# Performance work log

Hardware: AMD Instinct MI355X
Metric: run time of the kernel (lower is better)

## Reference

```python
import jax, jax.numpy as jnp
import numpy as np

B, S, D, H = 2, 2048, 1024, 16
DH = D // H


def setup_inputs() -> dict:
    key = jax.random.key(0)
    ks = jax.random.split(key, 5)
    scale = 0.02
    return {
        "X": jax.random.normal(ks[0], (B, S, D), jnp.float32),
        "Wq": jax.random.normal(ks[1], (H, D, DH), jnp.float32) * scale,
        "Wk": jax.random.normal(ks[2], (H, D, DH), jnp.float32) * scale,
        "Wv": jax.random.normal(ks[3], (H, D, DH), jnp.float32) * scale,
        "Wo": jax.random.normal(ks[4], (D, D), jnp.float32) * scale,
        "bo": jnp.zeros((D,), jnp.float32),
    }


def reference(X, Wq, Wk, Wv, Wo, bo):
    # Per-head projections, batched over heads: [B,H,S,DH]
    Q = jnp.einsum('bsd,hde->bhse', X, Wq)
    K = jnp.einsum('bsd,hde->bhse', X, Wk)
    V = jnp.einsum('bsd,hde->bhse', X, Wv)
    # Scores scaled by sqrt(d_model) exactly as in the source (not sqrt(d_head))
    A = jnp.einsum('bhse,bhte->bhst', Q, K) / jnp.sqrt(jnp.float32(D))
    A = jax.nn.softmax(A, axis=-1)  # no mask in the source
    O = jnp.einsum('bhst,bhte->bhse', A, V)  # [B,H,S,DH]
    # Concat heads -> [B,S,D], then output projection
    O = jnp.transpose(O, (0, 2, 1, 3)).reshape(B, S, D)
    return O @ Wo + bo
```

## Files before the change

### kernel.cpp

```cpp
#include <hip/hip_runtime.h>
#include <math.h>

static constexpr int Bc  = 2;
static constexpr int Sc  = 2048;
static constexpr int Dc  = 1024;
static constexpr int Hc  = 16;
static constexpr int DHc = 64;

typedef short bf16x8 __attribute__((ext_vector_type(8)));
typedef float f32x4  __attribute__((ext_vector_type(4)));

static constexpr float LOG2E = 1.4426950408889634f;

static __device__ __forceinline__ unsigned short f2bf(float x) {
  union { float f; unsigned u; } v; v.f = x;
  unsigned r = v.u + 0x7FFFu + ((v.u >> 16) & 1u);
  return (unsigned short)(r >> 16);
}
static __device__ __forceinline__ float bf2f(unsigned short u) {
  union { unsigned u; float f; } v; v.u = ((unsigned)u) << 16;
  return v.f;
}
static __device__ __forceinline__ unsigned pk2bf_trunc(float a, float b) {
  return __builtin_amdgcn_perm(__float_as_uint(b), __float_as_uint(a), 0x07060302u);
}
#if __has_builtin(__builtin_amdgcn_exp2f)
#define EXP2F(x) __builtin_amdgcn_exp2f(x)
#else
#define EXP2F(x) exp2f(x)
#endif

static __device__ __forceinline__ void gload16(const void* g, void* l) {
  __builtin_amdgcn_global_load_lds(
      (const __attribute__((address_space(1))) void*)g,
      (__attribute__((address_space(3))) void*)l, 16, 0, 0);
}

__global__ __launch_bounds__(256) void prep(
    const float* __restrict__ Wq, const float* __restrict__ Wk,
    const float* __restrict__ Wv, const float* __restrict__ Wo,
    const float* __restrict__ X,
    unsigned short* __restrict__ Wt3, unsigned short* __restrict__ Wot,
    unsigned short* __restrict__ Xb) {
  const int z = blockIdx.z;
  if (z == 4) {
    size_t base = ((size_t)blockIdx.y * 16 + blockIdx.x) * 4096;
#pragma unroll
    for (int it = 0; it < 16; ++it) {
      size_t i = base + it * 256 + threadIdx.x;
      float4 v = ((const float4*)X)[i];
      ushort4 u; u.x = f2bf(v.x); u.y = f2bf(v.y); u.z = f2bf(v.z); u.w = f2bf(v.w);
      ((ushort4*)Xb)[i] = u;
    }
    return;
  }
  __shared__ unsigned short T[64][68];
  const float* src; unsigned short* dst;
  int srcld, dstld, r0, c0;
  if (z < 3) {
    const float* W = (z == 0) ? Wq : (z == 1) ? Wk : Wv;
    unsigned short* Wt = Wt3 + (size_t)z * Dc * Dc;
    int h = blockIdx.y;
    src = W + (size_t)h * Dc * DHc;  srcld = DHc; r0 = blockIdx.x * 64; c0 = 0;
    dst = Wt + (size_t)h * DHc * Dc; dstld = Dc;
  } else {
    src = Wo;  srcld = Dc; r0 = blockIdx.x * 64; c0 = blockIdx.y * 64;
    dst = Wot; dstld = Dc;
  }
#pragma unroll
  for (int it = 0; it < 16; ++it) {
    int idx = it * 256 + threadIdx.x;
    int r = idx >> 6, c = idx & 63;
    T[c][r] = f2bf(src[(size_t)(r0 + r) * srcld + c0 + c]);
  }
  __syncthreads();
#pragma unroll
  for (int it = 0; it < 4; ++it) {
    int idx = it * 256 + threadIdx.x;
    int c = idx >> 4, r4 = (idx & 15) * 4;
    ushort4 u = *(const ushort4*)&T[c][r4];
    *(ushort4*)&dst[(size_t)(c0 + c) * dstld + r0 + r4] = u;
  }
}

__global__ __launch_bounds__(512, 2) void qkv_gemm(
    const unsigned short* __restrict__ Xb, const unsigned short* __restrict__ Wt3,
    unsigned short* __restrict__ Qb, unsigned short* __restrict__ Kb,
    unsigned short* __restrict__ Vtb) {
  __shared__ alignas(16) unsigned char smem[135168];
  unsigned short (*S)[64] = (unsigned short(*)[64])smem;

  const int tid = threadIdx.x;
  const int wv = tid >> 6, lane = tid & 63;
  const int ln = lane & 15, qd = (lane >> 4) & 3;
  const int wm = wv >> 2, wn = wv & 3;
  const int lr = lane >> 3;
  const int gcol = ((lane & 7) ^ lr) * 8;
  const int paq = ln & 7;

  const int bid = blockIdx.x;
  const int l = (bid & 7) * 24 + (bid >> 3);
  const int xb = l & 15, y = l >> 4;
  const int m0 = xb * 256, n0 = y * 256;
  const int which = y >> 2;
  const int b = m0 >> 11, s0 = m0 & 2047;
  const int h0 = (y & 3) * 4;

  const unsigned short* Ap = Xb + (size_t)m0 * 1024;
  const unsigned short* Bp = Wt3 + (size_t)n0 * 1024;
  const int grow = wv * 16 + lr;

#define STG(gb, srow) do {                                                  \
    gload16((gb) + (size_t)grow * 1024 + gcol,       &S[(srow) + wv * 16][0]); \
    gload16((gb) + (size_t)(grow + 8) * 1024 + gcol, &S[(srow) + wv * 16 + 8][0]); \
  } while (0)

#define RD_A(mh, rowbase) do {                                              \
    _Pragma("unroll") for (int mt = 0; mt < 4; ++mt)                        \
      _Pragma("unroll") for (int ks = 0; ks < 2; ++ks)                      \
        af[mt][ks] = *(const bf16x8*)&S[(rowbase) + (mh) * 64 + mt * 16 + ln] \
                                       [((ks * 4 + qd) ^ paq) * 8];         \
  } while (0)

#define RD_B(nh, rowbase) do {                                              \
    _Pragma("unroll") for (int nt = 0; nt < 2; ++nt)                        \
      _Pragma("unroll") for (int ks = 0; ks < 2; ++ks)                      \
        bf[(nh) * 2 + nt][ks] = *(const bf16x8*)&S[(rowbase) + (nh) * 32 + nt * 16 + ln] \
                                                  [((ks * 4 + qd) ^ paq) * 8]; \
  } while (0)

#define MM(mh, nh) do {                                                     \
    _Pragma("unroll") for (int ks = 0; ks < 2; ++ks)                        \
      _Pragma("unroll") for (int mt = 0; mt < 4; ++mt)                      \
        _Pragma("unroll") for (int nt = 0; nt < 2; ++nt)                    \
          acc[(mh) * 4 + mt][(nh) * 2 + nt] =                               \
              __builtin_amdgcn_mfma_f32_16x16x32_bf16(                      \
                  af[mt][ks], bf[(nh) * 2 + nt][ks],                        \
                  acc[(mh) * 4 + mt][(nh) * 2 + nt], 0, 0, 0);              \
  } while (0)

#define BAR __builtin_amdgcn_s_barrier()
#define WAITL asm volatile("s_waitcnt lgkmcnt(0)" ::: "memory")
#define WAITV(n) asm volatile("s_waitcnt vmcnt(" #n ")" ::: "memory")
#define PRIO1 __builtin_amdgcn_s_setprio(1)
#define PRIO0 __builtin_amdgcn_s_setprio(0)

  f32x4 acc[8][4];
#pragma unroll
  for (int mt = 0; mt < 8; ++mt)
#pragma unroll
    for (int nt = 0; nt < 4; ++nt) acc[mt][nt] = (f32x4){0.f, 0.f, 0.f, 0.f};

  STG(Bp, 512);
  STG(Ap, 0);
  STG(Ap + 128 * 1024, 128);
  STG(Bp + 128 * 1024, 640);
  STG(Bp + 64, 768);
  STG(Ap + 64, 256);
  WAITV(4);
  BAR;

  bf16x8 af[4][2], bf[4][2];

  for (int j = 0; j < 8; ++j) {
    const int last = (j == 7);
    const unsigned short* Ak = Ap + j * 128;
    const unsigned short* Bk = Bp + j * 128;

    STG(Ak + 128 * 1024 + 64, 384);
    RD_A(0, wm * 128);
    RD_B(0, 512 + (wn >> 1) * 128 + (wn & 1) * 64);
    BAR; WAITL;
    PRIO1; MM(0, 0); PRIO0; BAR;
    STG(Bk + 128 * 1024 + 64, 896);
    RD_B(1, 512 + (wn >> 1) * 128 + (wn & 1) * 64);
    BAR; WAITL;
    PRIO1; MM(0, 1); PRIO0; BAR;
    if (!last) STG(Bk + 128, 512);
    RD_A(1, wm * 128);
    BAR; WAITL;
    PRIO1; MM(1, 0); PRIO0; BAR;
    if (!last) STG(Ak + 128, 0);
    BAR;
    PRIO1; MM(1, 1); PRIO0;
    if (last) { WAITV(0); } else { WAITV(4); }
    BAR;

    if (!last) STG(Ak + 128 * 1024 + 128, 128);
    RD_A(0, 256 + wm * 128);
    RD_B(0, 768 + (wn >> 1) * 128 + (wn & 1) * 64);
    BAR; WAITL;
    PRIO1; MM(0, 0); PRIO0; BAR;
    if (!last) STG(Bk + 128 * 1024 + 128, 640);
    RD_B(1, 768 + (wn >> 1) * 128 + (wn & 1) * 64);
    BAR; WAITL;
    PRIO1; MM(0, 1); PRIO0; BAR;
    if (!last) STG(Bk + 192, 768);
    RD_A(1, 256 + wm * 128);
    BAR; WAITL;
    PRIO1; MM(1, 0); PRIO0; BAR;
    if (!last) STG(Ak + 192, 256);
    BAR;
    PRIO1; MM(1, 1); PRIO0;
    if (!last) WAITV(4);
    BAR;
  }

  unsigned short* Ts = (unsigned short*)smem;
  if (which < 2) {
    unsigned short* Out = (which == 0) ? Qb : Kb;
    const float scale = (which == 0) ? (LOG2E / 32.0f) : 1.0f;
#pragma unroll
    for (int mt = 0; mt < 8; ++mt)
#pragma unroll
      for (int nt = 0; nt < 4; ++nt)
#pragma unroll
        for (int r = 0; r < 4; ++r)
          Ts[(wm * 128 + mt * 16 + qd * 4 + r) * 264 + wn * 64 + nt * 16 + ln] =
              f2bf(acc[mt][nt][r] * scale);
    __syncthreads();
    const int row = tid >> 1;
#pragma unroll
    for (int it = 0; it < 16; ++it) {
      int c16 = (tid & 1) * 16 + it;
      int head = c16 >> 3, e8 = c16 & 7;
      *(ulonglong2*)&Out[(((size_t)b * Hc + h0 + head) * Sc + s0 + row) * DHc + e8 * 8] =
          *(const ulonglong2*)&Ts[row * 264 + c16 * 8];
    }
  } else {
#pragma unroll
    for (int mt = 0; mt < 8; ++mt)
#pragma unroll
      for (int nt = 0; nt < 4; ++nt)
#pragma unroll
        for (int r = 0; r < 4; ++r)
          Ts[(wn * 64 + nt * 16 + ln) * 264 + wm * 128 + mt * 16 + qd * 4 + r] =
              f2bf(acc[mt][nt][r]);
    __syncthreads();
    const int n = tid >> 1;
    const int head = n >> 6, e = n & 63;
    unsigned short* dst = Vtb + (((size_t)b * Hc + h0 + head) * DHc + e) * Sc + s0;
#pragma unroll
    for (int it = 0; it < 16; ++it) {
      int s16 = (tid & 1) * 16 + it;
      *(ulonglong2*)&dst[s16 * 8] = *(const ulonglong2*)&Ts[n * 264 + s16 * 8];
    }
  }
#undef STG
#undef RD_A
#undef RD_B
#undef MM
#undef BAR
#undef WAITL
#undef WAITV
#undef PRIO1
#undef PRIO0
}

__global__ __launch_bounds__(256, 2) void attn_partial(
    const unsigned short* __restrict__ Qb, const unsigned short* __restrict__ Kb,
    const unsigned short* __restrict__ Vtb,
    unsigned short* __restrict__ Opart, float* __restrict__ lpart) {
  __shared__ alignas(16) unsigned short Ks[64][64];
  __shared__ alignas(16) unsigned short Vts[64][64];
  __shared__ alignas(16) unsigned short Ps[256][64];

  const int tid = threadIdx.x;
  const int wv = tid >> 6, lane = tid & 63;
  const int ln = tid & 15, qd = (tid >> 4) & 3;
  const int sT = blockIdx.x, bh = blockIdx.y, sp = blockIdx.z;
  const int lr = lane >> 3;
  const int lcs = ((lane & 7) ^ lr) * 8;

  bf16x8 qf[4][2];
  const size_t qrow0 = (size_t)bh * Sc + sT * 256 + wv * 64;
#pragma unroll
  for (int mt = 0; mt < 4; ++mt)
#pragma unroll
    for (int ks = 0; ks < 2; ++ks)
      qf[mt][ks] = *(const bf16x8*)&Qb[(qrow0 + mt * 16 + ln) * DHc + ks * 32 + qd * 8];

  bf16x8 vones;
#pragma unroll
  for (int j = 0; j < 8; ++j) vones[j] = (short)0x3F80;

  f32x4 o[4][4], lacc[4];
#pragma unroll
  for (int mt = 0; mt < 4; ++mt) {
    lacc[mt] = (f32x4){0.f, 0.f, 0.f, 0.f};
#pragma unroll
    for (int et = 0; et < 4; ++et) o[mt][et] = (f32x4){0.f, 0.f, 0.f, 0.f};
  }

  for (int kb = sp * 16; kb < sp * 16 + 16; ++kb) {
    __syncthreads();
#pragma unroll
    for (int t = 0; t < 2; ++t) {
      gload16(Kb  + ((size_t)bh * Sc + kb * 64 + wv * 16 + t * 8 + lr) * DHc + lcs,
              &Ks[wv * 16 + t * 8][0]);
      gload16(Vtb + ((size_t)bh * DHc + wv * 16 + t * 8 + lr) * Sc + kb * 64 + lcs,
              &Vts[wv * 16 + t * 8][0]);
    }
    __syncthreads();

    f32x4 st[4][4];
#pragma unroll
    for (int mt = 0; mt < 4; ++mt)
#pragma unroll
      for (int nt = 0; nt < 4; ++nt) st[mt][nt] = (f32x4){0.f, 0.f, 0.f, 0.f};
#pragma unroll
    for (int ks = 0; ks < 2; ++ks) {
      const int pa = ((ks * 4 + qd) ^ (ln & 7)) * 8;
#pragma unroll
      for (int nt = 0; nt < 4; ++nt) {
        bf16x8 kf = *(const bf16x8*)&Ks[nt * 16 + ln][pa];
#pragma unroll
        for (int mt = 0; mt < 4; ++mt)
          st[mt][nt] = __builtin_amdgcn_mfma_f32_16x16x32_bf16(kf, qf[mt][ks], st[mt][nt], 0, 0, 0);
      }
    }

#pragma unroll
    for (int mt = 0; mt < 4; ++mt) {
      const int prow = wv * 64 + mt * 16 + ln;
#pragma unroll
      for (int nt = 0; nt < 4; ++nt) {
        float p0 = EXP2F(st[mt][nt][0]);
        float p1 = EXP2F(st[mt][nt][1]);
        float p2 = EXP2F(st[mt][nt][2]);
        float p3 = EXP2F(st[mt][nt][3]);
        uint2 w;
        w.x = pk2bf_trunc(p0, p1);
        w.y = pk2bf_trunc(p2, p3);
        int ppos = ((2 * nt + (qd >> 1)) ^ (ln & 7)) * 8 + (qd & 1) * 4;
        *(uint2*)&Ps[prow][ppos] = w;
      }
    }
    __syncthreads();

#pragma unroll
    for (int ks = 0; ks < 2; ++ks) {
      const int pa = ((ks * 4 + qd) ^ (ln & 7)) * 8;
      bf16x8 pf[4];
#pragma unroll
      for (int mt = 0; mt < 4; ++mt) {
        pf[mt] = *(const bf16x8*)&Ps[wv * 64 + mt * 16 + ln][pa];
        lacc[mt] = __builtin_amdgcn_mfma_f32_16x16x32_bf16(pf[mt], vones, lacc[mt], 0, 0, 0);
      }
#pragma unroll
      for (int et = 0; et < 4; ++et) {
        bf16x8 vf = *(const bf16x8*)&Vts[et * 16 + ln][pa];
#pragma unroll
        for (int mt = 0; mt < 4; ++mt)
          o[mt][et] = __builtin_amdgcn_mfma_f32_16x16x32_bf16(pf[mt], vf, o[mt][et], 0, 0, 0);
      }
    }
  }

  const size_t pbase = (size_t)sp * 65536 + ((size_t)bh * 8 + sT) * 256;
  if (ln == 0) {
#pragma unroll
    for (int mt = 0; mt < 4; ++mt)
#pragma unroll
      for (int r = 0; r < 4; ++r)
        lpart[pbase + wv * 64 + mt * 16 + qd * 4 + r] = lacc[mt][r];
  }
#pragma unroll
  for (int mt = 0; mt < 4; ++mt)
#pragma unroll
    for (int r = 0; r < 4; ++r) {
      int row = wv * 64 + mt * 16 + qd * 4 + r;
#pragma unroll
      for (int et = 0; et < 4; ++et)
        Opart[(pbase + row) * DHc + et * 16 + ln] = f2bf(o[mt][et][r]);
    }
}

__global__ __launch_bounds__(256) void out_gemm(
    const unsigned short* __restrict__ Opart, const float* __restrict__ lpart,
    const unsigned short* __restrict__ Wot,
    const float* __restrict__ bo, float* __restrict__ Out) {
  __shared__ alignas(16) unsigned short As[64][64];
  __shared__ alignas(16) unsigned short Bs[128][64];

  const int tid = threadIdx.x;
  const int wv = tid >> 6, lane = tid & 63;
  const int ln = tid & 15, qd = (tid >> 4) & 3;
  const int wm = wv >> 1, wn = wv & 1;
  const int m0 = blockIdx.x * 64, n0 = blockIdx.y * 128;
  const int lr = lane >> 3;
  const int lcs = ((lane & 7) ^ lr) * 8;

  f32x4 acc[2][4];
#pragma unroll
  for (int mt = 0; mt < 2; ++mt)
#pragma unroll
    for (int nt = 0; nt < 4; ++nt) acc[mt][nt] = (f32x4){0.f, 0.f, 0.f, 0.f};

  for (int k0 = 0; k0 < Dc; k0 += 64) {
    const int h = k0 >> 6;
    __syncthreads();
#pragma unroll
    for (int t = 0; t < 2; ++t) {
      const int arow = wv * 16 + t * 8 + lr;
      const int m = m0 + arow;
      const int b = m >> 11, s = m & 2047;
      const int sT = s >> 8, rr = s & 255;
      const size_t rbase = ((size_t)(b * Hc + h) * 8 + sT) * 256 + rr;
      ulonglong2 u0 = *(const ulonglong2*)&Opart[rbase * 64 + lcs];
      ulonglong2 u1 = *(const ulonglong2*)&Opart[(rbase + 65536) * 64 + lcs];
      const float inv = 1.0f / (lpart[rbase] + lpart[rbase + 65536]);
      const unsigned short* a0 = (const unsigned short*)&u0;
      const unsigned short* a1 = (const unsigned short*)&u1;
      uint4 w;
      unsigned d[4];
#pragma unroll
      for (int j = 0; j < 4; ++j) {
        unsigned short lo = f2bf((bf2f(a0[2 * j]) + bf2f(a1[2 * j])) * inv);
        unsigned short hi = f2bf((bf2f(a0[2 * j + 1]) + bf2f(a1[2 * j + 1])) * inv);
        d[j] = (unsigned)lo | ((unsigned)hi << 16);
      }
      w.x = d[0]; w.y = d[1]; w.z = d[2]; w.w = d[3];
      *(uint4*)&As[arow][(lane & 7) * 8] = w;
    }
#pragma unroll
    for (int t = 0; t < 4; ++t)
      gload16(Wot + (size_t)(n0 + wv * 32 + t * 8 + lr) * Dc + k0 + lcs, &Bs[wv * 32 + t * 8][0]);
    __syncthreads();
#pragma unroll
    for (int ks = 0; ks < 2; ++ks) {
      const int pa = ((ks * 4 + qd) ^ (ln & 7)) * 8;
      bf16x8 af[2], bf[4];
#pragma unroll
      for (int mt = 0; mt < 2; ++mt)
        af[mt] = *(const bf16x8*)&As[wm * 32 + mt * 16 + ln][pa];
#pragma unroll
      for (int nt = 0; nt < 4; ++nt)
        bf[nt] = *(const bf16x8*)&Bs[wn * 64 + nt * 16 + ln][pa];
#pragma unroll
      for (int mt = 0; mt < 2; ++mt)
#pragma unroll
        for (int nt = 0; nt < 4; ++nt)
          acc[mt][nt] = __builtin_amdgcn_mfma_f32_16x16x32_bf16(af[mt], bf[nt], acc[mt][nt], 0, 0, 0);
    }
  }

  float bias[4];
#pragma unroll
  for (int nt = 0; nt < 4; ++nt) bias[nt] = bo[n0 + wn * 64 + nt * 16 + ln];

#pragma unroll
  for (int mt = 0; mt < 2; ++mt)
#pragma unroll
    for (int r = 0; r < 4; ++r) {
      int m = m0 + wm * 32 + mt * 16 + qd * 4 + r;
#pragma unroll
      for (int nt = 0; nt < 4; ++nt)
        Out[(size_t)m * Dc + n0 + wn * 64 + nt * 16 + ln] = acc[mt][nt][r] + bias[nt];
    }
}

extern "C" void kernel_launch(void* const* d_in, const int* in_sizes, int n_in,
                              void* d_out, int out_size, void* d_ws, size_t ws_size,
                              hipStream_t stream) {
  (void)in_sizes; (void)n_in; (void)out_size; (void)ws_size;
  const float* X  = (const float*)d_in[0];
  const float* Wq = (const float*)d_in[1];
  const float* Wk = (const float*)d_in[2];
  const float* Wv = (const float*)d_in[3];
  const float* Wo = (const float*)d_in[4];
  const float* bo = (const float*)d_in[5];
  float* out = (float*)d_out;

  const size_t nX = (size_t)Bc * Sc * Dc;
  unsigned short* Xb    = (unsigned short*)d_ws;
  unsigned short* Wt3   = Xb + nX;
  unsigned short* Wot   = Wt3 + (size_t)3 * Dc * Dc;
  unsigned short* Qb    = Wot + (size_t)Dc * Dc;
  unsigned short* Kb    = Qb + nX;
  unsigned short* Vtb   = Kb + nX;
  unsigned short* Opart = Vtb + nX;
  float* lpart = (float*)(Opart + 2 * nX);

  prep<<<dim3(16, 16, 5), 256, 0, stream>>>(Wq, Wk, Wv, Wo, X, Wt3, Wot, Xb);
  qkv_gemm<<<dim3(192), 512, 0, stream>>>(Xb, Wt3, Qb, Kb, Vtb);
  attn_partial<<<dim3(8, 32, 2), 256, 0, stream>>>(Qb, Kb, Vtb, Opart, lpart);
  out_gemm<<<dim3(64, 8), 256, 0, stream>>>(Opart, lpart, Wot, bo, out);
}
```

Measured before the change: 187.6 us.

## Split attention keys three ways and double-buffer the output GEMM loads

The attention grid grows from two to three key splits (11/11/10 blocks of 64 keys), so 768 workgroups run instead of 512 and the GPU is filled better. The third partial and the row sums are written into workspace regions (Xb, Wt3) that are dead after the QKV GEMM. The output GEMM now double-buffers its LDS tiles, prefetching the next head's partials into registers and issuing the next weight tile while the current one is multiplied. The trade-offs are an extra partial to read and reduce, more registers, and reliance on hand-tuned vmcnt wait counts.

```diff
diff --git a/kernel.cpp b/kernel.cpp
--- a/kernel.cpp
+++ b/kernel.cpp
@@ -260,7 +260,8 @@
 __global__ __launch_bounds__(256, 2) void attn_partial(
     const unsigned short* __restrict__ Qb, const unsigned short* __restrict__ Kb,
     const unsigned short* __restrict__ Vtb,
-    unsigned short* __restrict__ Opart, float* __restrict__ lpart) {
+    unsigned short* __restrict__ Opart, unsigned short* __restrict__ Op2,
+    float* __restrict__ lp) {
   __shared__ alignas(16) unsigned short Ks[64][64];
   __shared__ alignas(16) unsigned short Vts[64][64];
   __shared__ alignas(16) unsigned short Ps[256][64];
@@ -272,6 +273,10 @@
   const int lr = lane >> 3;
   const int lcs = ((lane & 7) ^ lr) * 8;
 
+  const int kb0 = (sp == 0) ? 0 : (sp == 1) ? 11 : 22;
+  const int kb1 = (sp == 0) ? 11 : (sp == 1) ? 22 : 32;
+  unsigned short* Obase = (sp < 2) ? (Opart + (size_t)sp * 65536 * DHc) : Op2;
+
   bf16x8 qf[4][2];
   const size_t qrow0 = (size_t)bh * Sc + sT * 256 + wv * 64;
 #pragma unroll
@@ -292,7 +297,7 @@
     for (int et = 0; et < 4; ++et) o[mt][et] = (f32x4){0.f, 0.f, 0.f, 0.f};
   }
 
-  for (int kb = sp * 16; kb < sp * 16 + 16; ++kb) {
+  for (int kb = kb0; kb < kb1; ++kb) {
     __syncthreads();
 #pragma unroll
     for (int t = 0; t < 2; ++t) {
@@ -357,13 +362,13 @@
     }
   }
 
-  const size_t pbase = (size_t)sp * 65536 + ((size_t)bh * 8 + sT) * 256;
+  const size_t pbase = ((size_t)bh * 8 + sT) * 256;
   if (ln == 0) {
 #pragma unroll
     for (int mt = 0; mt < 4; ++mt)
 #pragma unroll
       for (int r = 0; r < 4; ++r)
-        lpart[pbase + wv * 64 + mt * 16 + qd * 4 + r] = lacc[mt][r];
+        lp[(size_t)sp * 65536 + pbase + wv * 64 + mt * 16 + qd * 4 + r] = lacc[mt][r];
   }
 #pragma unroll
   for (int mt = 0; mt < 4; ++mt)
@@ -372,16 +377,16 @@
       int row = wv * 64 + mt * 16 + qd * 4 + r;
 #pragma unroll
       for (int et = 0; et < 4; ++et)
-        Opart[(pbase + row) * DHc + et * 16 + ln] = f2bf(o[mt][et][r]);
+        Obase[(pbase + row) * DHc + et * 16 + ln] = f2bf(o[mt][et][r]);
     }
 }
 
 __global__ __launch_bounds__(256) void out_gemm(
-    const unsigned short* __restrict__ Opart, const float* __restrict__ lpart,
-    const unsigned short* __restrict__ Wot,
+    const unsigned short* __restrict__ Op01, const unsigned short* __restrict__ Op2,
+    const float* __restrict__ lp, const unsigned short* __restrict__ Wot,
     const float* __restrict__ bo, float* __restrict__ Out) {
-  __shared__ alignas(16) unsigned short As[64][64];
-  __shared__ alignas(16) unsigned short Bs[128][64];
+  __shared__ alignas(16) unsigned short As[2][64][64];
+  __shared__ alignas(16) unsigned short Bs[2][128][64];
 
   const int tid = threadIdx.x;
   const int wv = tid >> 6, lane = tid & 63;
@@ -391,57 +396,101 @@
   const int lr = lane >> 3;
   const int lcs = ((lane & 7) ^ lr) * 8;
 
+#define OBAR __builtin_amdgcn_s_barrier()
+#define OWAITL asm volatile("s_waitcnt lgkmcnt(0)" ::: "memory")
+#define OWAITV(n) asm volatile("s_waitcnt vmcnt(" #n ")" ::: "memory")
+
+  int rbase[2], arow[2];
+#pragma unroll
+  for (int t = 0; t < 2; ++t) {
+    arow[t] = wv * 16 + t * 8 + lr;
+    const int m = m0 + arow[t];
+    const int b = m >> 11, s = m & 2047;
+    rbase[t] = b * 32768 + (s >> 8) * 256 + (s & 255);
+  }
+
+  ulonglong2 pu0[2], pu1[2], pu2[2];
+  float pl0[2], pl1[2], pl2[2];
+
+#define LOADA(h) do {                                                        \
+    _Pragma("unroll") for (int t = 0; t < 2; ++t) {                          \
+      const size_t r = (size_t)rbase[t] + (h) * 2048;                        \
+      pu0[t] = *(const ulonglong2*)&Op01[r * 64 + lcs];                      \
+      pu1[t] = *(const ulonglong2*)&Op01[(r + 65536) * 64 + lcs];            \
+      pu2[t] = *(const ulonglong2*)&Op2[r * 64 + lcs];                       \
+      pl0[t] = lp[r]; pl1[t] = lp[r + 65536]; pl2[t] = lp[r + 131072];       \
+    }                                                                        \
+  } while (0)
+
+#define CONVA(buf) do {                                                      \
+    _Pragma("unroll") for (int t = 0; t < 2; ++t) {                          \
+      const float inv = 1.0f / (pl0[t] + pl1[t] + pl2[t]);                   \
+      const unsigned short* a0 = (const unsigned short*)&pu0[t];             \
+      const unsigned short* a1 = (const unsigned short*)&pu1[t];             \
+      const unsigned short* a2 = (const unsigned short*)&pu2[t];             \
+      unsigned d[4];                                                         \
+      _Pragma("unroll") for (int j = 0; j < 4; ++j) {                        \
+        unsigned short lo = f2bf((bf2f(a0[2 * j]) + bf2f(a1[2 * j]) +        \
+                                  bf2f(a2[2 * j])) * inv);                   \
+        unsigned short hi = f2bf((bf2f(a0[2 * j + 1]) + bf2f(a1[2 * j + 1]) + \
+                                  bf2f(a2[2 * j + 1])) * inv);               \
+        d[j] = (unsigned)lo | ((unsigned)hi << 16);                          \
+      }                                                                      \
+      uint4 w; w.x = d[0]; w.y = d[1]; w.z = d[2]; w.w = d[3];               \
+      *(uint4*)&As[(buf)][arow[t]][(lane & 7) * 8] = w;                      \
+    }                                                                        \
+  } while (0)
+
+#define GLOADB(h, buf) do {                                                  \
+    _Pragma("unroll") for (int t = 0; t < 4; ++t)                            \
+      gload16(Wot + (size_t)(n0 + wv * 32 + t * 8 + lr) * Dc + (h) * 64 + lcs, \
+              &Bs[(buf)][wv * 32 + t * 8][0]);                               \
+  } while (0)
+
   f32x4 acc[2][4];
 #pragma unroll
   for (int mt = 0; mt < 2; ++mt)
 #pragma unroll
     for (int nt = 0; nt < 4; ++nt) acc[mt][nt] = (f32x4){0.f, 0.f, 0.f, 0.f};
 
-  for (int k0 = 0; k0 < Dc; k0 += 64) {
-    const int h = k0 >> 6;
-    __syncthreads();
-#pragma unroll
-    for (int t = 0; t < 2; ++t) {
-      const int arow = wv * 16 + t * 8 + lr;
-      const int m = m0 + arow;
-      const int b = m >> 11, s = m & 2047;
-      const int sT = s >> 8, rr = s & 255;
-      const size_t rbase = ((size_t)(b * Hc + h) * 8 + sT) * 256 + rr;
-      ulonglong2 u0 = *(const ulonglong2*)&Opart[rbase * 64 + lcs];
-      ulonglong2 u1 = *(const ulonglong2*)&Opart[(rbase + 65536) * 64 + lcs];
-      const float inv = 1.0f / (lpart[rbase] + lpart[rbase + 65536]);
-      const unsigned short* a0 = (const unsigned short*)&u0;
-      const unsigned short* a1 = (const unsigned short*)&u1;
-      uint4 w;
-      unsigned d[4];
-#pragma unroll
-      for (int j = 0; j < 4; ++j) {
-        unsigned short lo = f2bf((bf2f(a0[2 * j]) + bf2f(a1[2 * j])) * inv);
-        unsigned short hi = f2bf((bf2f(a0[2 * j + 1]) + bf2f(a1[2 * j + 1])) * inv);
-        d[j] = (unsigned)lo | ((unsigned)hi << 16);
-      }
-      w.x = d[0]; w.y = d[1]; w.z = d[2]; w.w = d[3];
-      *(uint4*)&As[arow][(lane & 7) * 8] = w;
-    }
-#pragma unroll
-    for (int t = 0; t < 4; ++t)
-      gload16(Wot + (size_t)(n0 + wv * 32 + t * 8 + lr) * Dc + k0 + lcs, &Bs[wv * 32 + t * 8][0]);
-    __syncthreads();
+  GLOADB(0, 0);
+  LOADA(0);
+  CONVA(0);
+  LOADA(1);
+  OWAITV(0);
+  OWAITL;
+  OBAR;
+
+#pragma unroll
+  for (int k = 0; k < 16; ++k) {
+    const int cur = k & 1;
+    if (k < 15) GLOADB(k + 1, cur ^ 1);
+    if (k < 15) CONVA(cur ^ 1);
 #pragma unroll
     for (int ks = 0; ks < 2; ++ks) {
       const int pa = ((ks * 4 + qd) ^ (ln & 7)) * 8;
-      bf16x8 af[2], bf[4];
+      bf16x8 af[2], bfr[4];
 #pragma unroll
       for (int mt = 0; mt < 2; ++mt)
-        af[mt] = *(const bf16x8*)&As[wm * 32 + mt * 16 + ln][pa];
+        af[mt] = *(const bf16x8*)&As[cur][wm * 32 + mt * 16 + ln][pa];
 #pragma unroll
       for (int nt = 0; nt < 4; ++nt)
-        bf[nt] = *(const bf16x8*)&Bs[wn * 64 + nt * 16 + ln][pa];
+        bfr[nt] = *(const bf16x8*)&Bs[cur][wn * 64 + nt * 16 + ln][pa];
 #pragma unroll
       for (int mt = 0; mt < 2; ++mt)
 #pragma unroll
         for (int nt = 0; nt < 4; ++nt)
-          acc[mt][nt] = __builtin_amdgcn_mfma_f32_16x16x32_bf16(af[mt], bf[nt], acc[mt][nt], 0, 0, 0);
+          acc[mt][nt] = __builtin_amdgcn_mfma_f32_16x16x32_bf16(af[mt], bfr[nt], acc[mt][nt], 0, 0, 0);
+    }
+    if (k < 14) {
+      LOADA(k + 2);
+      OWAITV(12);
+      OWAITL;
+      OBAR;
+    } else if (k == 14) {
+      OWAITV(0);
+      OWAITL;
+      OBAR;
     }
   }
 
@@ -458,6 +507,12 @@
       for (int nt = 0; nt < 4; ++nt)
         Out[(size_t)m * Dc + n0 + wn * 64 + nt * 16 + ln] = acc[mt][nt][r] + bias[nt];
     }
+#undef LOADA
+#undef CONVA
+#undef GLOADB
+#undef OBAR
+#undef OWAITL
+#undef OWAITV
 }
 
 extern "C" void kernel_launch(void* const* d_in, const int* in_sizes, int n_in,
@@ -480,10 +535,11 @@
   unsigned short* Kb    = Qb + nX;
   unsigned short* Vtb   = Kb + nX;
   unsigned short* Opart = Vtb + nX;
-  float* lpart = (float*)(Opart + 2 * nX);
+  unsigned short* Op2   = Xb;
+  float* lp = (float*)Wt3;
 
   prep<<<dim3(16, 16, 5), 256, 0, stream>>>(Wq, Wk, Wv, Wo, X, Wt3, Wot, Xb);
   qkv_gemm<<<dim3(192), 512, 0, stream>>>(Xb, Wt3, Qb, Kb, Vtb);
-  attn_partial<<<dim3(8, 32, 2), 256, 0, stream>>>(Qb, Kb, Vtb, Opart, lpart);
-  out_gemm<<<dim3(64, 8), 256, 0, stream>>>(Opart, lpart, Wot, bo, out);
-}
+  attn_partial<<<dim3(8, 32, 3), 256, 0, stream>>>(Qb, Kb, Vtb, Opart, Op2, lp);
+  out_gemm<<<dim3(64, 8), 256, 0, stream>>>(Opart, Op2, lp, Wot, bo, out);
+}
```

Measured after the change: 194.4 us. 1.04x slower.
